# Kernel optimization log

Measured on AMD Instinct MI355X. Metric: run time of the kernel, lower is better.

Reference implementation:

```python
import jax, jax.numpy as jnp
import numpy as np

N, P, D_IN, K, D_H = 4, 20000, 1024, 8, 64


def setup_inputs() -> dict:
    key = jax.random.key(0)
    ks = jax.random.split(key, 10)
    inp = {
        "x": jax.random.normal(ks[0], (N, P, D_IN), dtype=jnp.float32),
        "centroids": jax.random.normal(ks[1], (K, D_IN), dtype=jnp.float32),
        # proj_pre: Linear(in_dim, 64) + ReLU  (W stored as [in, out])
        "W_pre": jax.random.normal(ks[2], (D_IN, D_H), dtype=jnp.float32) / np.sqrt(D_IN),
        "b_pre": jnp.zeros((D_H,), dtype=jnp.float32),
        # attention: Linear(64,32) -> Tanh -> Linear(32,1)
        "W_a1": jax.random.normal(ks[3], (D_H, 32), dtype=jnp.float32) / np.sqrt(D_H),
        "b_a1": jnp.zeros((32,), dtype=jnp.float32),
        "W_a2": jax.random.normal(ks[4], (32, 1), dtype=jnp.float32) / np.sqrt(32.0),
        "b_a2": jnp.zeros((1,), dtype=jnp.float32),
        # proj_out: Linear(64,32) + ReLU (+ Dropout, identity at eval)
        "W_out": jax.random.normal(ks[5], (D_H, 32), dtype=jnp.float32) / np.sqrt(D_H),
        "b_out": jnp.zeros((32,), dtype=jnp.float32),
    }
    return inp


def reference(x, centroids, W_pre, b_pre, W_a1, b_a1, W_a2, b_a2, W_out, b_out):
    # --- cdist-based hard cluster assignment ---------------------------------
    # ||x - c||: use the expanded form to avoid an [n,p,K,d] broadcast.
    x2 = jnp.sum(x * x, axis=-1)                       # [n, p]
    c2 = jnp.sum(centroids * centroids, axis=-1)       # [K]
    d2 = x2[..., None] + c2 - 2.0 * jnp.einsum('npd,kd->npk', x, centroids)
    dist = jnp.sqrt(jnp.maximum(d2, 0.0))              # [n, p, K]

    wc = jax.nn.softmax(1e7 / dist, axis=-1)           # softmax(1e7/dist)
    wc = (wc > 0.5).astype(x.dtype)                    # hard assignment
    # F.normalize(p=1, dim=1): divide by per-(n,K) patch count (eps=1e-12)
    wc = wc / jnp.maximum(jnp.sum(wc, axis=1, keepdims=True), 1e-12)
    mask = jnp.sum(wc, axis=1) == 0                    # [n, K] empty clusters

    # --- per-patch projection -------------------------------------------------
    xp = jax.nn.relu(x @ W_pre + b_pre)                # [n, p, 64]

    # --- cluster pooling + attention ------------------------------------------
    x_cls = jnp.einsum('npd,nph->nhd', xp, wc)         # [n, K, 64]
    A = (jnp.tanh(x_cls @ W_a1 + b_a1) @ W_a2 + b_a2)[..., 0]  # [n, K]
    A = jnp.where(mask, jnp.asarray(-100000.0, A.dtype), A)
    wa = jax.nn.softmax(A, axis=-1)                    # [n, K]
    pooled = jnp.einsum('nhd,nh->nd', x_cls, wa)       # [n, 64]

    enc_cls = jax.nn.relu(pooled @ W_out + b_out)      # [n, 32] (dropout = eval)
    enc_seq = xp.reshape(-1, xp.shape[-1])             # [(n*p), 64]
    return enc_cls, enc_seq, enc_seq
```

## Files before the change

kernel.cpp:

```cpp
#include <hip/hip_runtime.h>
#include <math.h>

#define N_  4
#define P_  20000
#define DIN 1024
#define K_  8
#define DH  64
#define BP  64
#define BD  64
#define XS  68


__global__ __launch_bounds__(512) void k_init(const float* __restrict__ centroids,
                                              float* __restrict__ ws) {
  const int t = threadIdx.x;
  float* gsum = ws;
  int*   gcnt = (int*)(ws + 2048);
  float* c2   = ws + 2080;
  for (int i = t; i < N_ * K_ * DH; i += 512) gsum[i] = 0.f;
  if (t < N_ * K_) gcnt[t] = 0;
  const int w = t >> 6, lane = t & 63;
  float s = 0.f;
  for (int d = lane; d < DIN; d += 64) {
    float v = centroids[w * DIN + d];
    s += v * v;
  }
  for (int off = 32; off > 0; off >>= 1) s += __shfl_down(s, off, 64);
  if (lane == 0) c2[w] = s;
}

__global__ __launch_bounds__(256) void k_main(
    const float* __restrict__ x, const float* __restrict__ centroids,
    const float* __restrict__ W_pre, const float* __restrict__ b_pre,
    float* __restrict__ out1, float* __restrict__ out2, float* __restrict__ ws) {
  __shared__ float xt[BP * XS];
  __shared__ float wt[BD * DH];
  __shared__ float ct[K_ * XS];
  __shared__ float sdist[BP * 9];
  __shared__ int   assign_s[BP];
  __shared__ int   cnt8[K_];

  const int t  = threadIdx.x;
  const int n  = blockIdx.y;
  const int p0 = blockIdx.x * BP;
  const int tx = t & 15;
  const int tz = (t >> 4) & 3;
  const int w  = t >> 6;
  const int jb = 16 * w + 4 * tz;

  float* gsum = ws;
  int*   gcnt = (int*)(ws + 2048);
  const float* c2 = ws + 2080;

  for (int i = t; i < BP * 9; i += 256) sdist[i] = 0.f;
  if (t < K_) cnt8[t] = 0;

  float acc[4][4];
#pragma unroll
  for (int i = 0; i < 4; ++i)
#pragma unroll
    for (int jj = 0; jj < 4; ++jj) acc[i][jj] = 0.f;

  const int r  = t >> 4;
  const int c4 = (t & 15) << 2;

  for (int d0 = 0; d0 < DIN; d0 += BD) {
    __syncthreads();
#pragma unroll
    for (int rr = 0; rr < 4; ++rr) {
      const int p = r + 16 * rr;
      float4 v = make_float4(0.f, 0.f, 0.f, 0.f);
      if (p0 + p < P_)
        v = *(const float4*)&x[(size_t)(n * P_ + p0 + p) * DIN + d0 + c4];
      *(float4*)&xt[p * XS + c4] = v;
    }
#pragma unroll
    for (int rr = 0; rr < 4; ++rr) {
      const int d = r + 16 * rr;
      *(float4*)&wt[d * DH + c4] = *(const float4*)&W_pre[(size_t)(d0 + d) * DH + c4];
    }
    if (t < 128) {
      const int k = t >> 4;
      *(float4*)&ct[k * XS + c4] = *(const float4*)&centroids[(size_t)k * DIN + d0 + c4];
    }
    __syncthreads();

    for (int dd = 0; dd < BD; dd += 4) {
      float xv[4][4], wv[4][4];
#pragma unroll
      for (int i = 0; i < 4; ++i)
        *(float4*)&xv[i][0] = *(const float4*)&xt[(tx + 16 * i) * XS + dd];
#pragma unroll
      for (int q = 0; q < 4; ++q)
        *(float4*)&wv[q][0] = *(const float4*)&wt[(dd + q) * DH + jb];
#pragma unroll
      for (int i = 0; i < 4; ++i)
#pragma unroll
        for (int jj = 0; jj < 4; ++jj)
#pragma unroll
          for (int q = 0; q < 4; ++q)
            acc[i][jj] += xv[i][q] * wv[q][jj];
    }

    for (int task = t; task < BP * 9; task += 256) {
      const int p = task / 9;
      const int k = task - 9 * p;
      const float* a = &xt[p * XS];
      const float* b = (k < 8) ? &ct[k * XS] : a;
      float s = 0.f;
#pragma unroll
      for (int dd = 0; dd < BD; dd += 4) {
        float4 av = *(const float4*)&a[dd];
        float4 bv = *(const float4*)&b[dd];
        s += av.x * bv.x + av.y * bv.y + av.z * bv.z + av.w * bv.w;
      }
      sdist[task] += s;
    }
  }
  __syncthreads();

  if (t < BP) {
    int a = -1;
    if (p0 + t < P_) {
      const float x2 = sdist[t * 9 + 8];
      float best = 3.4e38f;
      int bk = 0;
#pragma unroll
      for (int k = 0; k < K_; ++k) {
        const float d2 = x2 + c2[k] - 2.f * sdist[t * 9 + k];
        if (d2 < best) { best = d2; bk = k; }
      }
      a = bk;
      atomicAdd(&cnt8[bk], 1);
    }
    assign_s[t] = a;
  }

  const float4 bp4 = *(const float4*)&b_pre[jb];
  const float bpf[4] = {bp4.x, bp4.y, bp4.z, bp4.w};
#pragma unroll
  for (int i = 0; i < 4; ++i) {
    const int p = tx + 16 * i;
    float v[4];
#pragma unroll
    for (int jj = 0; jj < 4; ++jj) {
      const float u = acc[i][jj] + bpf[jj];
      v[jj] = u > 0.f ? u : 0.f;
    }
    *(float4*)&xt[p * XS + jb] = *(const float4*)v;
    if (p0 + p < P_) {
      const size_t o = (size_t)(n * P_ + p0 + p) * DH + jb;
      *(float4*)&out1[o] = *(const float4*)v;
      *(float4*)&out2[o] = *(const float4*)v;
    }
  }
  __syncthreads();

  for (int task = t; task < K_ * DH; task += 256) {
    const int k = task >> 6;
    const int j = task & 63;
    float s = 0.f;
    for (int p = 0; p < BP; ++p)
      s += (assign_s[p] == k) ? xt[p * XS + j] : 0.f;
    if (s != 0.f) atomicAdd(&gsum[(n * K_ + k) * DH + j], s);
  }
  if (t < K_ && cnt8[t] > 0) atomicAdd(&gcnt[n * K_ + t], cnt8[t]);
}

__global__ __launch_bounds__(256) void k_final(
    const float* __restrict__ W_a1, const float* __restrict__ b_a1,
    const float* __restrict__ W_a2, const float* __restrict__ b_a2,
    const float* __restrict__ W_out, const float* __restrict__ b_out,
    const float* __restrict__ ws, float* __restrict__ enc_cls) {
  __shared__ float xc[N_ * K_ * DH];
  __shared__ float wa[N_ * K_];
  __shared__ float As[N_ * K_];
  __shared__ int   cnts[N_ * K_];
  __shared__ float pooled[N_ * DH];
  const int t = threadIdx.x;
  const float* gsum = ws;
  const int* gcnt = (const int*)(ws + 2048);

  if (t < N_ * K_) cnts[t] = gcnt[t];
  __syncthreads();
  for (int i = t; i < N_ * K_ * DH; i += 256) {
    const int nk = i >> 6;
    const int c = cnts[nk];
    xc[i] = (c > 0) ? gsum[i] / (float)c : 0.f;
  }
  __syncthreads();
  if (t < N_ * K_) {
    float a = b_a2[0];
    for (int h = 0; h < 32; ++h) {
      float z = b_a1[h];
      for (int j = 0; j < DH; ++j) z += xc[t * DH + j] * W_a1[j * 32 + h];
      a += tanhf(z) * W_a2[h];
    }
    As[t] = (cnts[t] > 0) ? a : -100000.f;
  }
  __syncthreads();
  if (t < N_) {
    float m = -3.4e38f;
    for (int k = 0; k < K_; ++k) m = fmaxf(m, As[t * K_ + k]);
    float ssum = 0.f;
    float e[K_];
    for (int k = 0; k < K_; ++k) { e[k] = expf(As[t * K_ + k] - m); ssum += e[k]; }
    for (int k = 0; k < K_; ++k) wa[t * K_ + k] = e[k] / ssum;
  }
  __syncthreads();
  {
    const int n = t >> 6, j = t & 63;
    float s = 0.f;
    for (int k = 0; k < K_; ++k) s += xc[(n * K_ + k) * DH + j] * wa[n * K_ + k];
    pooled[t] = s;
  }
  __syncthreads();
  if (t < N_ * 32) {
    const int n = t >> 5, o = t & 31;
    float s = b_out[o];
    for (int j = 0; j < DH; ++j) s += pooled[n * DH + j] * W_out[j * 32 + o];
    enc_cls[n * 32 + o] = fmaxf(s, 0.f);
  }
}

extern "C" void kernel_launch(void* const* d_in, const int* in_sizes, int n_in,
                              void* d_out, int out_size, void* d_ws, size_t ws_size,
                              hipStream_t stream) {
  const float* x         = (const float*)d_in[0];
  const float* centroids = (const float*)d_in[1];
  const float* W_pre     = (const float*)d_in[2];
  const float* b_pre     = (const float*)d_in[3];
  const float* W_a1      = (const float*)d_in[4];
  const float* b_a1      = (const float*)d_in[5];
  const float* W_a2      = (const float*)d_in[6];
  const float* b_a2      = (const float*)d_in[7];
  const float* W_out     = (const float*)d_in[8];
  const float* b_out     = (const float*)d_in[9];

  float* out     = (float*)d_out;
  float* ws      = (float*)d_ws;
  float* enc_cls = out;
  float* out1    = out + N_ * 32;
  float* out2    = out + N_ * 32 + (size_t)N_ * P_ * DH;

  hipLaunchKernelGGL(k_init, dim3(1), dim3(512), 0, stream, centroids, ws);
  hipLaunchKernelGGL(k_main, dim3((P_ + BP - 1) / BP, N_), dim3(256), 0, stream,
                     x, centroids, W_pre, b_pre, out1, out2, ws);
  hipLaunchKernelGGL(k_final, dim3(1), dim3(256), 0, stream,
                     W_a1, b_a1, W_a2, b_a2, W_out, b_out, ws, enc_cls);
}
```

Baseline: 644.8 us.

## Use split-bf16 MFMA for projection and centroid dot products

Replaces the scalar FP32 register-tiled GEMM with bf16 MFMA 16x16x32 instructions. Each fp32 operand is split into high and low bf16 parts, and three products are accumulated to keep near-fp32 accuracy. A prep kernel pre-splits and transposes W_pre and the centroids into bf16 arrays in the workspace, with the centroids added as an extra column tile so the distance dot products come out of the same MFMAs. The patch tile grows to 128 rows and the x-squared term is dropped from the argmin. The split-bf16 scheme carries some rounding risk that could flip near-tie cluster assignments.

```diff
diff --git a/kernel.cpp b/kernel.cpp
--- a/kernel.cpp
+++ b/kernel.cpp
@@ -6,165 +6,193 @@
 #define DIN 1024
 #define K_  8
 #define DH  64
-#define BP  64
-#define BD  64
-#define XS  68
-
-
-__global__ __launch_bounds__(512) void k_init(const float* __restrict__ centroids,
+#define BP  128
+#define NT  5
+
+typedef float  f32x4 __attribute__((ext_vector_type(4)));
+typedef short  s16x8 __attribute__((ext_vector_type(8)));
+typedef unsigned int u32x4 __attribute__((ext_vector_type(4)));
+typedef unsigned short ushort_t;
+
+
+union FragU { u32x4 u; s16x8 s; };
+
+__global__ __launch_bounds__(256) void k_prep(const float* __restrict__ W_pre,
+                                              const float* __restrict__ centroids,
                                               float* __restrict__ ws) {
-  const int t = threadIdx.x;
-  float* gsum = ws;
-  int*   gcnt = (int*)(ws + 2048);
-  float* c2   = ws + 2080;
-  for (int i = t; i < N_ * K_ * DH; i += 512) gsum[i] = 0.f;
+  const int c = blockIdx.x;
+  const int t = threadIdx.x;
+  ushort_t* Bth = (ushort_t*)(ws + 4096);
+  ushort_t* Btl = (ushort_t*)(ws + 45056);
+  for (int d = t; d < DIN; d += 256) {
+    float v = 0.f;
+    if (c < 64)      v = W_pre[(size_t)d * DH + c];
+    else if (c < 72) v = centroids[(size_t)(c - 64) * DIN + d];
+    unsigned u = __float_as_uint(v);
+    unsigned r = u + 0x7FFFu + ((u >> 16) & 1u);
+    unsigned hb = r & 0xFFFF0000u;
+    float lo = v - __uint_as_float(hb);
+    unsigned ul = __float_as_uint(lo);
+    unsigned rl = ul + 0x7FFFu + ((ul >> 16) & 1u);
+    Bth[(size_t)c * DIN + d] = (ushort_t)(hb >> 16);
+    Btl[(size_t)c * DIN + d] = (ushort_t)(rl >> 16);
+  }
+}
+
+__global__ __launch_bounds__(512) void k_init2(const float* __restrict__ centroids,
+                                               float* __restrict__ ws) {
+  const int t = threadIdx.x;
+  int* gcnt = (int*)(ws + 2048);
+  for (int i = t; i < N_ * K_ * DH; i += 512) ws[i] = 0.f;
   if (t < N_ * K_) gcnt[t] = 0;
   const int w = t >> 6, lane = t & 63;
   float s = 0.f;
   for (int d = lane; d < DIN; d += 64) {
-    float v = centroids[w * DIN + d];
+    float v = centroids[(size_t)w * DIN + d];
     s += v * v;
   }
   for (int off = 32; off > 0; off >>= 1) s += __shfl_down(s, off, 64);
-  if (lane == 0) c2[w] = s;
+  if (lane == 0) ws[2080 + w] = s;
 }
 
 __global__ __launch_bounds__(256) void k_main(
-    const float* __restrict__ x, const float* __restrict__ centroids,
-    const float* __restrict__ W_pre, const float* __restrict__ b_pre,
+    const float* __restrict__ x, const float* __restrict__ b_pre,
     float* __restrict__ out1, float* __restrict__ out2, float* __restrict__ ws) {
-  __shared__ float xt[BP * XS];
-  __shared__ float wt[BD * DH];
-  __shared__ float ct[K_ * XS];
-  __shared__ float sdist[BP * 9];
+  __shared__ float xt[BP * 68];
+  __shared__ float sc[BP * 9];
   __shared__ int   assign_s[BP];
   __shared__ int   cnt8[K_];
-
-  const int t  = threadIdx.x;
-  const int n  = blockIdx.y;
+  __shared__ float c2s[K_];
+
+  const int t = threadIdx.x;
+  const int w = t >> 6, l = t & 63;
+  const int n = blockIdx.y;
   const int p0 = blockIdx.x * BP;
-  const int tx = t & 15;
-  const int tz = (t >> 4) & 3;
-  const int w  = t >> 6;
-  const int jb = 16 * w + 4 * tz;
-
-  float* gsum = ws;
-  int*   gcnt = (int*)(ws + 2048);
-  const float* c2 = ws + 2080;
-
-  for (int i = t; i < BP * 9; i += 256) sdist[i] = 0.f;
-  if (t < K_) cnt8[t] = 0;
-
-  float acc[4][4];
-#pragma unroll
-  for (int i = 0; i < 4; ++i)
-#pragma unroll
-    for (int jj = 0; jj < 4; ++jj) acc[i][jj] = 0.f;
-
-  const int r  = t >> 4;
-  const int c4 = (t & 15) << 2;
-
-  for (int d0 = 0; d0 < DIN; d0 += BD) {
+  const int validP = (P_ - p0) < BP ? (P_ - p0) : BP;
+
+  const ushort_t* Bth = (const ushort_t*)(ws + 4096);
+  const ushort_t* Btl = (const ushort_t*)(ws + 45056);
+
+  if (t < K_) { cnt8[t] = 0; c2s[t] = ws[2080 + t]; }
+
+  f32x4 acc[2][NT];
+#pragma unroll
+  for (int rg = 0; rg < 2; ++rg)
+#pragma unroll
+    for (int tl = 0; tl < NT; ++tl) acc[rg][tl] = (f32x4){0.f, 0.f, 0.f, 0.f};
+
+  const float* xbase = x + (size_t)n * P_ * DIN;
+  const int quad8 = (l >> 4) << 3;
+
+  for (int ch = 0; ch < 16; ++ch) {
+    const int d0 = ch * 64;
     __syncthreads();
 #pragma unroll
-    for (int rr = 0; rr < 4; ++rr) {
-      const int p = r + 16 * rr;
-      float4 v = make_float4(0.f, 0.f, 0.f, 0.f);
-      if (p0 + p < P_)
-        v = *(const float4*)&x[(size_t)(n * P_ + p0 + p) * DIN + d0 + c4];
-      *(float4*)&xt[p * XS + c4] = v;
-    }
-#pragma unroll
-    for (int rr = 0; rr < 4; ++rr) {
-      const int d = r + 16 * rr;
-      *(float4*)&wt[d * DH + c4] = *(const float4*)&W_pre[(size_t)(d0 + d) * DH + c4];
-    }
-    if (t < 128) {
-      const int k = t >> 4;
-      *(float4*)&ct[k * XS + c4] = *(const float4*)&centroids[(size_t)k * DIN + d0 + c4];
+    for (int i = 0; i < 8; ++i) {
+      const int idx = t + 256 * i;
+      const int row = idx >> 4, c4 = (idx & 15) << 2;
+      int gp = p0 + row; gp = gp < P_ ? gp : P_ - 1;
+      f32x4 v = *(const f32x4*)(xbase + (size_t)gp * DIN + d0 + c4);
+      *(f32x4*)(xt + row * 68 + c4) = v;
     }
     __syncthreads();
 
-    for (int dd = 0; dd < BD; dd += 4) {
-      float xv[4][4], wv[4][4];
-#pragma unroll
-      for (int i = 0; i < 4; ++i)
-        *(float4*)&xv[i][0] = *(const float4*)&xt[(tx + 16 * i) * XS + dd];
-#pragma unroll
-      for (int q = 0; q < 4; ++q)
-        *(float4*)&wv[q][0] = *(const float4*)&wt[(dd + q) * DH + jb];
-#pragma unroll
-      for (int i = 0; i < 4; ++i)
-#pragma unroll
-        for (int jj = 0; jj < 4; ++jj)
-#pragma unroll
-          for (int q = 0; q < 4; ++q)
-            acc[i][jj] += xv[i][q] * wv[q][jj];
-    }
-
-    for (int task = t; task < BP * 9; task += 256) {
-      const int p = task / 9;
-      const int k = task - 9 * p;
-      const float* a = &xt[p * XS];
-      const float* b = (k < 8) ? &ct[k * XS] : a;
-      float s = 0.f;
-#pragma unroll
-      for (int dd = 0; dd < BD; dd += 4) {
-        float4 av = *(const float4*)&a[dd];
-        float4 bv = *(const float4*)&b[dd];
-        s += av.x * bv.x + av.y * bv.y + av.z * bv.z + av.w * bv.w;
-      }
-      sdist[task] += s;
-    }
+#pragma unroll
+    for (int kk = 0; kk < 2; ++kk) {
+      const int kb = d0 + kk * 32 + quad8;
+      FragU bh[NT], bl[NT];
+#pragma unroll
+      for (int tl = 0; tl < NT; ++tl) {
+        const size_t off = (size_t)(tl * 16 + (l & 15)) * DIN + kb;
+        bh[tl].u = *(const u32x4*)(Bth + off);
+        bl[tl].u = *(const u32x4*)(Btl + off);
+      }
+#pragma unroll
+      for (int rg = 0; rg < 2; ++rg) {
+        const int row = 32 * w + 16 * rg + (l & 15);
+        const float* ap = xt + row * 68 + kk * 32 + quad8;
+        f32x4 a0 = *(const f32x4*)ap;
+        f32x4 a1 = *(const f32x4*)(ap + 4);
+        float f[8];
+#pragma unroll
+        for (int e = 0; e < 4; ++e) { f[e] = a0[e]; f[4 + e] = a1[e]; }
+        FragU ah, al;
+#pragma unroll
+        for (int q = 0; q < 4; ++q) {
+          const unsigned u0 = __float_as_uint(f[2 * q]);
+          const unsigned u1 = __float_as_uint(f[2 * q + 1]);
+          ah.u[q] = (u0 >> 16) | (u1 & 0xFFFF0000u);
+          const float l0 = f[2 * q]     - __uint_as_float(u0 & 0xFFFF0000u);
+          const float l1 = f[2 * q + 1] - __uint_as_float(u1 & 0xFFFF0000u);
+          al.u[q] = (__float_as_uint(l0) >> 16) | (__float_as_uint(l1) & 0xFFFF0000u);
+        }
+#pragma unroll
+        for (int tl = 0; tl < NT; ++tl) {
+          acc[rg][tl] = __builtin_amdgcn_mfma_f32_16x16x32_bf16(ah.s, bh[tl].s, acc[rg][tl], 0, 0, 0);
+          acc[rg][tl] = __builtin_amdgcn_mfma_f32_16x16x32_bf16(ah.s, bl[tl].s, acc[rg][tl], 0, 0, 0);
+          acc[rg][tl] = __builtin_amdgcn_mfma_f32_16x16x32_bf16(al.s, bh[tl].s, acc[rg][tl], 0, 0, 0);
+        }
+      }
+    }
+  }
+  __syncthreads();
+
+#pragma unroll
+  for (int tl = 0; tl < 4; ++tl) {
+    const int col = tl * 16 + (l & 15);
+    const float bb = b_pre[col];
+#pragma unroll
+    for (int rg = 0; rg < 2; ++rg) {
+#pragma unroll
+      for (int r = 0; r < 4; ++r) {
+        const int row = 32 * w + 16 * rg + ((l >> 4) << 2) + r;
+        float v = acc[rg][tl][r] + bb;
+        v = v > 0.f ? v : 0.f;
+        xt[row * 65 + col] = v;
+        if (row < validP) {
+          const size_t o = (((size_t)(n * P_ + p0 + row)) << 6) + col;
+          out1[o] = v;
+          out2[o] = v;
+        }
+      }
+    }
+  }
+  if ((l & 15) < K_) {
+    const int k = l & 15;
+#pragma unroll
+    for (int rg = 0; rg < 2; ++rg)
+#pragma unroll
+      for (int r = 0; r < 4; ++r) {
+        const int row = 32 * w + 16 * rg + ((l >> 4) << 2) + r;
+        sc[row * 9 + k] = c2s[k] - 2.f * acc[rg][4][r];
+      }
   }
   __syncthreads();
 
   if (t < BP) {
     int a = -1;
-    if (p0 + t < P_) {
-      const float x2 = sdist[t * 9 + 8];
-      float best = 3.4e38f;
-      int bk = 0;
+    if (t < validP) {
+      float best = 3.4e38f; int bk = 0;
 #pragma unroll
       for (int k = 0; k < K_; ++k) {
-        const float d2 = x2 + c2[k] - 2.f * sdist[t * 9 + k];
-        if (d2 < best) { best = d2; bk = k; }
+        const float v = sc[t * 9 + k];
+        if (v < best) { best = v; bk = k; }
       }
       a = bk;
       atomicAdd(&cnt8[bk], 1);
     }
     assign_s[t] = a;
   }
-
-  const float4 bp4 = *(const float4*)&b_pre[jb];
-  const float bpf[4] = {bp4.x, bp4.y, bp4.z, bp4.w};
-#pragma unroll
-  for (int i = 0; i < 4; ++i) {
-    const int p = tx + 16 * i;
-    float v[4];
-#pragma unroll
-    for (int jj = 0; jj < 4; ++jj) {
-      const float u = acc[i][jj] + bpf[jj];
-      v[jj] = u > 0.f ? u : 0.f;
-    }
-    *(float4*)&xt[p * XS + jb] = *(const float4*)v;
-    if (p0 + p < P_) {
-      const size_t o = (size_t)(n * P_ + p0 + p) * DH + jb;
-      *(float4*)&out1[o] = *(const float4*)v;
-      *(float4*)&out2[o] = *(const float4*)v;
-    }
-  }
   __syncthreads();
 
   for (int task = t; task < K_ * DH; task += 256) {
-    const int k = task >> 6;
-    const int j = task & 63;
+    const int k = task >> 6, j = task & 63;
     float s = 0.f;
     for (int p = 0; p < BP; ++p)
-      s += (assign_s[p] == k) ? xt[p * XS + j] : 0.f;
-    if (s != 0.f) atomicAdd(&gsum[(n * K_ + k) * DH + j], s);
-  }
-  if (t < K_ && cnt8[t] > 0) atomicAdd(&gcnt[n * K_ + t], cnt8[t]);
+      s += (assign_s[p] == k) ? xt[p * 65 + j] : 0.f;
+    if (s != 0.f) atomicAdd(&ws[(n * K_ + k) * DH + j], s);
+  }
+  if (t < K_ && cnt8[t] > 0) atomicAdd((int*)(ws + 2048) + n * K_ + t, cnt8[t]);
 }
 
 __global__ __launch_bounds__(256) void k_final(
@@ -243,9 +271,10 @@
   float* out1    = out + N_ * 32;
   float* out2    = out + N_ * 32 + (size_t)N_ * P_ * DH;
 
-  hipLaunchKernelGGL(k_init, dim3(1), dim3(512), 0, stream, centroids, ws);
+  hipLaunchKernelGGL(k_prep, dim3(80), dim3(256), 0, stream, W_pre, centroids, ws);
+  hipLaunchKernelGGL(k_init2, dim3(1), dim3(512), 0, stream, centroids, ws);
   hipLaunchKernelGGL(k_main, dim3((P_ + BP - 1) / BP, N_), dim3(256), 0, stream,
-                     x, centroids, W_pre, b_pre, out1, out2, ws);
+                     x, b_pre, out1, out2, ws);
   hipLaunchKernelGGL(k_final, dim3(1), dim3(256), 0, stream,
                      W_a1, b_a1, W_a2, b_a2, W_out, b_out, ws, enc_cls);
 }
```

New measurement: 620.1 us. 1.04x faster.
